# Performance work log

Measured on AMD Instinct MI355X. Metric: run time of the kernel, lower is better.

The kernel has to match this reference:

```python
import jax, jax.numpy as jnp
import numpy as np

N_PAPER, N_AUTHOR = 50000, 20000
D_IN, D_HID, N_CLS = 128, 128, 40
E_WRITES, E_CITES, E_REV = 400000, 800000, 400000
ETS = ["w", "c", "r"]  # writes(author->paper), cites(paper->paper), rev_writes(paper->author)


def setup_inputs() -> dict:
    key = jax.random.key(0)
    keys = iter(jax.random.split(key, 64))

    def nrm(shape, scale=1.0):
        return jax.random.normal(next(keys), shape, jnp.float32) * scale

    inp = {}
    inp["x_paper"] = nrm((N_PAPER, D_IN))
    inp["x_author"] = nrm((N_AUTHOR, D_IN))

    def edges(n_src, n_dst, e):
        return jnp.stack([
            jax.random.randint(next(keys), (e,), 0, n_src),
            jax.random.randint(next(keys), (e,), 0, n_dst),
        ]).astype(jnp.int32)

    inp["ei_writes"] = edges(N_AUTHOR, N_PAPER, E_WRITES)
    inp["ei_cites"] = edges(N_PAPER, N_PAPER, E_CITES)
    inp["ei_rev"] = edges(N_PAPER, N_AUTHOR, E_REV)

    # SAGEConv params per layer, per relation: W_l (neighbor lin, with bias), W_r (root lin)
    dims = [(D_IN, D_HID), (D_HID, N_CLS)]
    for l, (di, do) in enumerate(dims):
        s = 1.0 / float(np.sqrt(di))
        for e in ETS:
            inp[f"Wl{l}_{e}"] = nrm((di, do), s)
            inp[f"bl{l}_{e}"] = jnp.zeros((do,), jnp.float32)
            inp[f"Wr{l}_{e}"] = nrm((di, do), s)
    return inp


def _sage(x_src, x_dst, ei, Wl, bl, Wr, n_dst):
    # PyG SAGEConv(aggr='mean'): lin_l(mean of neighbor msgs) + lin_r(x_dst)
    msg = x_src[ei[0]]                                                    # [E, d]
    s = jax.ops.segment_sum(msg, ei[1], num_segments=n_dst)               # [n_dst, d]
    cnt = jax.ops.segment_sum(jnp.ones((ei.shape[1],), msg.dtype), ei[1],
                              num_segments=n_dst)
    agg = s / jnp.maximum(cnt, 1.0)[:, None]
    return agg @ Wl + bl + x_dst @ Wr


def reference(x_paper, x_author, ei_writes, ei_cites, ei_rev,
              Wl0_w, bl0_w, Wr0_w, Wl0_c, bl0_c, Wr0_c, Wl0_r, bl0_r, Wr0_r,
              Wl1_w, bl1_w, Wr1_w, Wl1_c, bl1_c, Wr1_c, Wl1_r, bl1_r, Wr1_r):
    def layer(hp, ha, Pw, Pc, Pr):
        out_w = _sage(ha, hp, ei_writes, *Pw, N_PAPER)   # author -> paper
        out_c = _sage(hp, hp, ei_cites, *Pc, N_PAPER)    # paper  -> paper
        out_a = _sage(hp, ha, ei_rev, *Pr, N_AUTHOR)     # paper  -> author
        # HeteroConv aggr='mean': average over relations sharing a dst type
        return 0.5 * (out_w + out_c), out_a

    hp, ha = layer(x_paper, x_author,
                   (Wl0_w, bl0_w, Wr0_w), (Wl0_c, bl0_c, Wr0_c), (Wl0_r, bl0_r, Wr0_r))
    hp, ha = jax.nn.relu(hp), jax.nn.relu(ha)  # dropout is identity at eval
    hp, ha = layer(hp, ha,
                   (Wl1_w, bl1_w, Wr1_w), (Wl1_c, bl1_c, Wr1_c), (Wl1_r, bl1_r, Wr1_r))
    return hp
```

## Files before the change

### kernel.cpp

```cpp
#include <hip/hip_runtime.h>

#define NP 50000
#define NA 20000
#define EW 400000
#define EC 800000
#define ER 400000

__global__ __launch_bounds__(256) void prep_k(
    const float* __restrict__ Wr0w, const float* __restrict__ Wr0c,
    const float* __restrict__ bl0w, const float* __restrict__ bl0c,
    const float* __restrict__ Wr1w, const float* __restrict__ Wr1c,
    const float* __restrict__ bl1w, const float* __restrict__ bl1c,
    float* __restrict__ Wr0wc, float* __restrict__ b0p,
    float* __restrict__ Wr1wc, float* __restrict__ b1p)
{
    int i = blockIdx.x * 256 + threadIdx.x;
    if (i < 128*128) Wr0wc[i] = Wr0w[i] + Wr0c[i];
    if (i < 128*40)  Wr1wc[i] = Wr1w[i] + Wr1c[i];
    if (i < 128)     b0p[i] = 0.5f*(bl0w[i] + bl0c[i]);
    if (i < 40)      b1p[i] = 0.5f*(bl1w[i] + bl1c[i]);
}

__global__ __launch_bounds__(256) void count_all_k(
    const int* __restrict__ ei_w, const int* __restrict__ ei_c, const int* __restrict__ ei_r,
    int* __restrict__ cntw, int* __restrict__ cntc, int* __restrict__ cntr)
{
    int i = blockIdx.x * 256 + threadIdx.x;
    if (i < EW)              atomicAdd(&cntw[ei_w[EW + i]], 1);
    else if (i < EW+EC)      atomicAdd(&cntc[ei_c[EC + (i-EW)]], 1);
    else if (i < EW+EC+ER)   atomicAdd(&cntr[ei_r[ER + (i-EW-EC)]], 1);
}

__global__ __launch_bounds__(1024) void scan3_k(
    int* __restrict__ c0, int n0, int* __restrict__ o0,
    int* __restrict__ c1, int n1, int* __restrict__ o1,
    int* __restrict__ c2, int n2, int* __restrict__ o2)
{
    __shared__ int sa[1024], sb[1024];
    __shared__ int carry_s;
    int* cnt; int n; int* off;
    if (blockIdx.x == 0)      { cnt = c0; n = n0; off = o0; }
    else if (blockIdx.x == 1) { cnt = c1; n = n1; off = o1; }
    else                      { cnt = c2; n = n2; off = o2; }
    const int tid = threadIdx.x;
    if (tid == 0) carry_s = 0;
    __syncthreads();
    const int nchunk = (n + 1023) / 1024;
    for (int c = 0; c < nchunk; ++c) {
        int i = c*1024 + tid;
        int v = (i < n) ? cnt[i] : 0;
        sa[tid] = v;
        __syncthreads();
        int* s = sa; int* d = sb;
        for (int sh = 1; sh < 1024; sh <<= 1) {
            int t = s[tid] + ((tid >= sh) ? s[tid - sh] : 0);
            d[tid] = t;
            __syncthreads();
            int* tmp = s; s = d; d = tmp;
        }
        int inc = s[tid];
        int carry = carry_s;
        if (i < n) off[i] = carry + inc - v;
        __syncthreads();
        if (tid == 1023) carry_s = carry + inc;
        __syncthreads();
    }
    if (tid == 0) off[n] = carry_s;
}

__global__ __launch_bounds__(256) void fill_all_k(
    const int* __restrict__ ei_w, const int* __restrict__ ei_c, const int* __restrict__ ei_r,
    const int* __restrict__ offw, const int* __restrict__ offc, const int* __restrict__ offr,
    int* __restrict__ cntw, int* __restrict__ cntc, int* __restrict__ cntr,
    int* __restrict__ adjw, int* __restrict__ adjc, int* __restrict__ adjr)
{
    int i = blockIdx.x * 256 + threadIdx.x;
    const int* ei; const int* off; int* cnt; int* adj; int e; int E;
    if (i < EW)            { e = i;        ei = ei_w; off = offw; cnt = cntw; adj = adjw; E = EW; }
    else if (i < EW+EC)    { e = i-EW;     ei = ei_c; off = offc; cnt = cntc; adj = adjc; E = EC; }
    else if (i < EW+EC+ER) { e = i-EW-EC;  ei = ei_r; off = offr; cnt = cntr; adj = adjr; E = ER; }
    else return;
    int d = ei[E + e];
    int p = atomicSub(&cnt[d], 1) - 1;
    adj[off[d] + p] = ei[e];
}

__global__ __launch_bounds__(256) void gather128_all_k(
    const float* __restrict__ x_paper, const float* __restrict__ x_author,
    const int* __restrict__ offw, const int* __restrict__ adjw, float* __restrict__ aggw,
    const int* __restrict__ offc, const int* __restrict__ adjc, float* __restrict__ aggc,
    const int* __restrict__ offr, const int* __restrict__ adjr, float* __restrict__ aggr)
{
    int W    = blockIdx.x * 4 + (threadIdx.x >> 6);
    int lane = threadIdx.x & 63;
    const float* X; const int* off; const int* adj; float* AGG; int w;
    if (W < NP)          { w = W;        X = x_author; off = offw; adj = adjw; AGG = aggw; }
    else if (W < 2*NP)   { w = W - NP;   X = x_paper;  off = offc; adj = adjc; AGG = aggc; }
    else if (W < 2*NP+NA){ w = W - 2*NP; X = x_paper;  off = offr; adj = adjr; AGG = aggr; }
    else return;
    int b = off[w], e = off[w+1];
    float2 acc = make_float2(0.f, 0.f);
    for (int j0 = b; j0 < e; j0 += 64) {
        int sl = (j0 + lane < e) ? adj[j0 + lane] : 0;
        int m  = min(64, e - j0);
        for (int k = 0; k < m; ++k) {
            int s = __shfl(sl, k, 64);
            float2 v = reinterpret_cast<const float2*>(X + (size_t)s * 128)[lane];
            acc.x += v.x; acc.y += v.y;
        }
    }
    float sc = 1.0f / fmaxf((float)(e - b), 1.0f);
    reinterpret_cast<float2*>(AGG + (size_t)w * 128)[lane] = make_float2(acc.x*sc, acc.y*sc);
}

__device__ __forceinline__ void fma4(float4& c, float a, const float4& b) {
    c.x += a*b.x; c.y += a*b.y; c.z += a*b.z; c.w += a*b.w;
}

__global__ __launch_bounds__(256) void gemmf_k(
    const float* __restrict__ A0, const float* __restrict__ A1, const float* __restrict__ A2,
    const float* __restrict__ B0, const float* __restrict__ B1, const float* __restrict__ B2,
    float* __restrict__ C, int M, int nparts, float alpha,
    const float* __restrict__ bias, int relu)
{
    __shared__ float As[32][128];
    __shared__ float Bs[32][128];
    const int tid  = threadIdx.x;
    const int row0 = blockIdx.x * 128;
    const int tx = tid & 15;
    const int ty = tid >> 4;

    float4 acc[2][2][4];
#pragma unroll
    for (int rh = 0; rh < 2; ++rh)
#pragma unroll
        for (int ch = 0; ch < 2; ++ch)
#pragma unroll
            for (int i = 0; i < 4; ++i) acc[rh][ch][i] = make_float4(0.f,0.f,0.f,0.f);

    const int KT = nparts * 4;
    for (int kt = 0; kt < KT; ++kt) {
        const int p  = kt >> 2;
        const int cb = (kt & 3) * 32;
        const float* Ap = (p == 0) ? A0 : (p == 1) ? A1 : A2;
        const float* Bp = (p == 0) ? B0 : (p == 1) ? B1 : B2;
        if (kt) __syncthreads();
#pragma unroll
        for (int i = 0; i < 4; ++i) {
            int idx = tid + i*256;
            int m = idx & 127, kq = idx >> 7;
            int row = row0 + m;
            float4 v = make_float4(0.f,0.f,0.f,0.f);
            if (row < M) v = *reinterpret_cast<const float4*>(Ap + (size_t)row*128 + cb + kq*4);
            As[kq*4+0][m] = v.x; As[kq*4+1][m] = v.y;
            As[kq*4+2][m] = v.z; As[kq*4+3][m] = v.w;
        }
#pragma unroll
        for (int i = 0; i < 4; ++i) {
            int idx = tid + i*256;
            int n4 = idx & 31, k = idx >> 5;
            *reinterpret_cast<float4*>(&Bs[k][n4*4]) =
                *reinterpret_cast<const float4*>(Bp + (size_t)(cb + k)*128 + n4*4);
        }
        __syncthreads();
#pragma unroll 8
        for (int k = 0; k < 32; ++k) {
            float4 a0 = *reinterpret_cast<const float4*>(&As[k][ty*4]);
            float4 a1 = *reinterpret_cast<const float4*>(&As[k][64 + ty*4]);
            float4 b0 = *reinterpret_cast<const float4*>(&Bs[k][tx*4]);
            float4 b1 = *reinterpret_cast<const float4*>(&Bs[k][64 + tx*4]);
#pragma unroll
            for (int i = 0; i < 4; ++i) {
                float av = (&a0.x)[i];
                fma4(acc[0][0][i], av, b0);
                fma4(acc[0][1][i], av, b1);
            }
#pragma unroll
            for (int i = 0; i < 4; ++i) {
                float av = (&a1.x)[i];
                fma4(acc[1][0][i], av, b0);
                fma4(acc[1][1][i], av, b1);
            }
        }
    }

#pragma unroll
    for (int rh = 0; rh < 2; ++rh)
#pragma unroll
        for (int i = 0; i < 4; ++i) {
            int row = row0 + rh*64 + ty*4 + i;
            if (row >= M) continue;
#pragma unroll
            for (int ch = 0; ch < 2; ++ch) {
                int col = ch*64 + tx*4;
                float4 t = acc[rh][ch][i];
                float4 bb = *reinterpret_cast<const float4*>(&bias[col]);
                t.x = alpha*t.x + bb.x; t.y = alpha*t.y + bb.y;
                t.z = alpha*t.z + bb.z; t.w = alpha*t.w + bb.w;
                if (relu) {
                    t.x = fmaxf(t.x, 0.f); t.y = fmaxf(t.y, 0.f);
                    t.z = fmaxf(t.z, 0.f); t.w = fmaxf(t.w, 0.f);
                }
                *reinterpret_cast<float4*>(C + (size_t)row*128 + col) = t;
            }
        }
}

__global__ __launch_bounds__(256) void gemm40_k(
    const float* __restrict__ A, const float* __restrict__ B, float* __restrict__ C, int M)
{
    __shared__ float Bs[128][40];
    __shared__ float As[24][128];
    const int tid  = threadIdx.x;
    const int row0 = blockIdx.x * 24;

#pragma unroll
    for (int i = 0; i < 5; ++i) {
        int idx = tid + i*256;
        reinterpret_cast<float4*>(&Bs[0][0])[idx] = reinterpret_cast<const float4*>(B)[idx];
    }
#pragma unroll
    for (int i = 0; i < 3; ++i) {
        int idx = tid + i*256;
        int r = idx >> 5, c4 = idx & 31;
        int row = row0 + r;
        float4 v = make_float4(0.f,0.f,0.f,0.f);
        if (row < M) v = reinterpret_cast<const float4*>(A + (size_t)row*128)[c4];
        reinterpret_cast<float4*>(&As[r][0])[c4] = v;
    }
    __syncthreads();

    if (tid < 240) {
        int col  = tid % 40;
        int rsub = tid / 40;
        float a0=0.f, a1=0.f, a2=0.f, a3=0.f;
        for (int k = 0; k < 128; ++k) {
            float b = Bs[k][col];
            a0 += As[rsub*4+0][k]*b;
            a1 += As[rsub*4+1][k]*b;
            a2 += As[rsub*4+2][k]*b;
            a3 += As[rsub*4+3][k]*b;
        }
        int rb = row0 + rsub*4;
        if (rb+0 < M) C[(size_t)(rb+0)*40 + col] = a0;
        if (rb+1 < M) C[(size_t)(rb+1)*40 + col] = a1;
        if (rb+2 < M) C[(size_t)(rb+2)*40 + col] = a2;
        if (rb+3 < M) C[(size_t)(rb+3)*40 + col] = a3;
    }
}

__global__ __launch_bounds__(256) void gemm40x2_k(
    const float* __restrict__ A, const float* __restrict__ B1, const float* __restrict__ B2,
    float* __restrict__ C1, float* __restrict__ C2, int M)
{
    __shared__ float Bs1[128][40];
    __shared__ float Bs2[128][40];
    __shared__ float As[24][128];
    const int tid  = threadIdx.x;
    const int row0 = blockIdx.x * 24;

#pragma unroll
    for (int i = 0; i < 5; ++i) {
        int idx = tid + i*256;
        reinterpret_cast<float4*>(&Bs1[0][0])[idx] = reinterpret_cast<const float4*>(B1)[idx];
        reinterpret_cast<float4*>(&Bs2[0][0])[idx] = reinterpret_cast<const float4*>(B2)[idx];
    }
#pragma unroll
    for (int i = 0; i < 3; ++i) {
        int idx = tid + i*256;
        int r = idx >> 5, c4 = idx & 31;
        int row = row0 + r;
        float4 v = make_float4(0.f,0.f,0.f,0.f);
        if (row < M) v = reinterpret_cast<const float4*>(A + (size_t)row*128)[c4];
        reinterpret_cast<float4*>(&As[r][0])[c4] = v;
    }
    __syncthreads();

    if (tid < 240) {
        int col  = tid % 40;
        int rsub = tid / 40;
        float p0=0.f,p1=0.f,p2=0.f,p3=0.f;
        float q0=0.f,q1=0.f,q2=0.f,q3=0.f;
        for (int k = 0; k < 128; ++k) {
            float b1 = Bs1[k][col];
            float b2 = Bs2[k][col];
            float v0 = As[rsub*4+0][k], v1 = As[rsub*4+1][k];
            float v2 = As[rsub*4+2][k], v3 = As[rsub*4+3][k];
            p0 += v0*b1; p1 += v1*b1; p2 += v2*b1; p3 += v3*b1;
            q0 += v0*b2; q1 += v1*b2; q2 += v2*b2; q3 += v3*b2;
        }
        int rb = row0 + rsub*4;
        if (rb+0 < M) { C1[(size_t)(rb+0)*40 + col] = p0; C2[(size_t)(rb+0)*40 + col] = q0; }
        if (rb+1 < M) { C1[(size_t)(rb+1)*40 + col] = p1; C2[(size_t)(rb+1)*40 + col] = q1; }
        if (rb+2 < M) { C1[(size_t)(rb+2)*40 + col] = p2; C2[(size_t)(rb+2)*40 + col] = q2; }
        if (rb+3 < M) { C1[(size_t)(rb+3)*40 + col] = p3; C2[(size_t)(rb+3)*40 + col] = q3; }
    }
}

__global__ __launch_bounds__(256) void gather40f_k(
    const float* __restrict__ T1w, const float* __restrict__ T1c,
    const int* __restrict__ offw, const int* __restrict__ adjw,
    const int* __restrict__ offc, const int* __restrict__ adjc,
    const float* __restrict__ b1p, float* __restrict__ out)
{
    int w    = blockIdx.x * 4 + (threadIdx.x >> 6);
    int lane = threadIdx.x & 63;
    if (w >= NP) return;
    const bool act = lane < 40;

    float aw = 0.f;
    {
        int b = offw[w], e = offw[w+1];
        for (int j0 = b; j0 < e; j0 += 64) {
            int sl = (j0 + lane < e) ? adjw[j0 + lane] : 0;
            int m  = min(64, e - j0);
            for (int k = 0; k < m; ++k) {
                int s = __shfl(sl, k, 64);
                if (act) aw += T1w[(size_t)s * 40 + lane];
            }
        }
        aw *= 1.0f / fmaxf((float)(e - b), 1.0f);
    }
    float ac = 0.f;
    {
        int b = offc[w], e = offc[w+1];
        for (int j0 = b; j0 < e; j0 += 64) {
            int sl = (j0 + lane < e) ? adjc[j0 + lane] : 0;
            int m  = min(64, e - j0);
            for (int k = 0; k < m; ++k) {
                int s = __shfl(sl, k, 64);
                if (act) ac += T1c[(size_t)s * 40 + lane];
            }
        }
        ac *= 1.0f / fmaxf((float)(e - b), 1.0f);
    }
    if (act) {
        size_t idx = (size_t)w * 40 + lane;
        out[idx] = 0.5f*(aw + ac + out[idx]) + b1p[lane];
    }
}

extern "C" void kernel_launch(void* const* d_in, const int* in_sizes, int n_in,
                              void* d_out, int out_size, void* d_ws, size_t ws_size,
                              hipStream_t stream)
{
    (void)in_sizes; (void)n_in; (void)out_size; (void)ws_size;

    const float* x_paper  = (const float*)d_in[0];
    const float* x_author = (const float*)d_in[1];
    const int*   ei_w     = (const int*)d_in[2];
    const int*   ei_c     = (const int*)d_in[3];
    const int*   ei_r     = (const int*)d_in[4];
    const float* Wl0w = (const float*)d_in[5];
    const float* bl0w = (const float*)d_in[6];
    const float* Wr0w = (const float*)d_in[7];
    const float* Wl0c = (const float*)d_in[8];
    const float* bl0c = (const float*)d_in[9];
    const float* Wr0c = (const float*)d_in[10];
    const float* Wl0r = (const float*)d_in[11];
    const float* bl0r = (const float*)d_in[12];
    const float* Wr0r = (const float*)d_in[13];
    const float* Wl1w = (const float*)d_in[14];
    const float* bl1w = (const float*)d_in[15];
    const float* Wr1w = (const float*)d_in[16];
    const float* Wl1c = (const float*)d_in[17];
    const float* bl1c = (const float*)d_in[18];
    const float* Wr1c = (const float*)d_in[19];
    float* out = (float*)d_out;

    float* ws = (float*)d_ws;
    size_t o = 0;
    int* cntw = (int*)(ws + o); o += NP;
    int* cntc = (int*)(ws + o); o += NP;
    int* cntr = (int*)(ws + o); o += NA;
    const size_t zeroInts = o;
    int* offw = (int*)(ws + o); o += NP + 1;
    int* offc = (int*)(ws + o); o += NP + 1;
    int* offr = (int*)(ws + o); o += NA + 1;
    o = (o + 3) & ~(size_t)3;
    int* adjw = (int*)(ws + o); o += EW;
    int* adjc = (int*)(ws + o); o += EC;
    int* adjr = (int*)(ws + o); o += ER;
    float* aggw = ws + o; o += (size_t)NP*128;
    float* aggc = ws + o; o += (size_t)NP*128;
    float* aggr = ws + o; o += (size_t)NA*128;
    float* hp1  = ws + o; o += (size_t)NP*128;
    float* ha1  = ws + o; o += (size_t)NA*128;
    float* Wr0wc = ws + o; o += 128*128;
    float* b0p   = ws + o; o += 128;
    float* Wr1wc = ws + o; o += 128*40;
    float* b1p   = ws + o; o += 40;
    float* T1w   = aggw;
    float* T1c   = aggw + (size_t)NA*40;

    hipMemsetAsync(d_ws, 0, zeroInts * sizeof(int), stream);

    prep_k<<<64, 256, 0, stream>>>(Wr0w, Wr0c, bl0w, bl0c, Wr1w, Wr1c, bl1w, bl1c,
                                   Wr0wc, b0p, Wr1wc, b1p);

    count_all_k<<<(EW+EC+ER+255)/256, 256, 0, stream>>>(ei_w, ei_c, ei_r, cntw, cntc, cntr);
    scan3_k<<<3, 1024, 0, stream>>>(cntw, NP, offw, cntc, NP, offc, cntr, NA, offr);
    fill_all_k<<<(EW+EC+ER+255)/256, 256, 0, stream>>>(ei_w, ei_c, ei_r, offw, offc, offr,
                                                       cntw, cntc, cntr, adjw, adjc, adjr);

    gather128_all_k<<<(2*NP+NA+3)/4, 256, 0, stream>>>(x_paper, x_author,
                                                       offw, adjw, aggw,
                                                       offc, adjc, aggc,
                                                       offr, adjr, aggr);

    gemmf_k<<<(NP+127)/128, 256, 0, stream>>>(x_paper, aggw, aggc, Wr0wc, Wl0w, Wl0c,
                                              hp1, NP, 3, 0.5f, b0p, 1);
    gemmf_k<<<(NA+127)/128, 256, 0, stream>>>(x_author, aggr, nullptr, Wr0r, Wl0r, nullptr,
                                              ha1, NA, 2, 1.0f, bl0r, 1);

    gemm40_k  <<<(NA+23)/24, 256, 0, stream>>>(ha1, Wl1w, T1w, NA);
    gemm40x2_k<<<(NP+23)/24, 256, 0, stream>>>(hp1, Wl1c, Wr1wc, T1c, out, NP);

    gather40f_k<<<(NP+3)/4, 256, 0, stream>>>(T1w, T1c, offw, adjw, offc, adjc, b1p, out);
}
```

Before: 721.1 us.

## Use wave-shuffle scan in CSR offsets and register-prefetch GEMM tiles

The single-block-per-relation prefix scan now handles 4096 elements per chunk with int4 loads, wave-level shuffle scans and a small cross-wave scan. This replaces the 10-step shared-memory Hillis-Steele scan that synchronized the block at every step. Offset arrays are padded so that vector stores stay 16-byte aligned. The dense GEMM now prefetches the next k-tile from global memory into registers while computing the current tile, which hides load latency at the cost of extra registers and an extra barrier.

```diff
diff --git a/kernel.cpp b/kernel.cpp
--- a/kernel.cpp
+++ b/kernel.cpp
@@ -32,37 +32,66 @@
 }
 
 __global__ __launch_bounds__(1024) void scan3_k(
-    int* __restrict__ c0, int n0, int* __restrict__ o0,
-    int* __restrict__ c1, int n1, int* __restrict__ o1,
-    int* __restrict__ c2, int n2, int* __restrict__ o2)
-{
-    __shared__ int sa[1024], sb[1024];
+    const int* __restrict__ c0, int n0, int* __restrict__ o0,
+    const int* __restrict__ c1, int n1, int* __restrict__ o1,
+    const int* __restrict__ c2, int n2, int* __restrict__ o2)
+{
+    __shared__ int wsum[16];
     __shared__ int carry_s;
-    int* cnt; int n; int* off;
+    const int* cnt; int n; int* off;
     if (blockIdx.x == 0)      { cnt = c0; n = n0; off = o0; }
     else if (blockIdx.x == 1) { cnt = c1; n = n1; off = o1; }
     else                      { cnt = c2; n = n2; off = o2; }
-    const int tid = threadIdx.x;
+    const int tid  = threadIdx.x;
+    const int lane = tid & 63;
+    const int wid  = tid >> 6;
     if (tid == 0) carry_s = 0;
     __syncthreads();
-    const int nchunk = (n + 1023) / 1024;
+    const int CH = 4096;
+    const int nchunk = (n + CH - 1) / CH;
     for (int c = 0; c < nchunk; ++c) {
-        int i = c*1024 + tid;
-        int v = (i < n) ? cnt[i] : 0;
-        sa[tid] = v;
+        int base = c*CH + tid*4;
+        int4 v = make_int4(0,0,0,0);
+        if (base + 3 < n) v = *reinterpret_cast<const int4*>(cnt + base);
+        else {
+            if (base   < n) v.x = cnt[base];
+            if (base+1 < n) v.y = cnt[base+1];
+            if (base+2 < n) v.z = cnt[base+2];
+            if (base+3 < n) v.w = cnt[base+3];
+        }
+        int s1 = v.x + v.y, s2 = s1 + v.z, s3 = s2 + v.w;
+        int x = s3;
+#pragma unroll
+        for (int d = 1; d < 64; d <<= 1) {
+            int u = __shfl_up(x, d, 64);
+            if (lane >= d) x += u;
+        }
+        if (lane == 63) wsum[wid] = x;
+        int texc = x - s3;
         __syncthreads();
-        int* s = sa; int* d = sb;
-        for (int sh = 1; sh < 1024; sh <<= 1) {
-            int t = s[tid] + ((tid >= sh) ? s[tid - sh] : 0);
-            d[tid] = t;
-            __syncthreads();
-            int* tmp = s; s = d; d = tmp;
-        }
-        int inc = s[tid];
+        if (wid == 0 && lane < 16) {
+            int y = wsum[lane];
+#pragma unroll
+            for (int d = 1; d < 16; d <<= 1) {
+                int u = __shfl_up(y, d, 16);
+                if (lane >= d) y += u;
+            }
+            wsum[lane] = y;
+        }
+        __syncthreads();
         int carry = carry_s;
-        if (i < n) off[i] = carry + inc - v;
+        int wexc  = wid ? wsum[wid-1] : 0;
+        int pre   = carry + wexc + texc;
+        int4 ov = make_int4(pre, pre + v.x, pre + s1, pre + s2);
+        if (base + 3 < n) *reinterpret_cast<int4*>(off + base) = ov;
+        else {
+            if (base   < n) off[base]   = ov.x;
+            if (base+1 < n) off[base+1] = ov.y;
+            if (base+2 < n) off[base+2] = ov.z;
+            if (base+3 < n) off[base+3] = ov.w;
+        }
         __syncthreads();
-        if (tid == 1023) carry_s = carry + inc;
+        if (tid == 0) carry_s += wsum[15];
         __syncthreads();
     }
     if (tid == 0) off[n] = carry_s;
@@ -139,30 +168,41 @@
             for (int i = 0; i < 4; ++i) acc[rh][ch][i] = make_float4(0.f,0.f,0.f,0.f);
 
     const int KT = nparts * 4;
-    for (int kt = 0; kt < KT; ++kt) {
+    float4 ra[4], rb[4];
+
+    auto loadT = [&](int kt) {
         const int p  = kt >> 2;
         const int cb = (kt & 3) * 32;
         const float* Ap = (p == 0) ? A0 : (p == 1) ? A1 : A2;
         const float* Bp = (p == 0) ? B0 : (p == 1) ? B1 : B2;
-        if (kt) __syncthreads();
 #pragma unroll
         for (int i = 0; i < 4; ++i) {
             int idx = tid + i*256;
             int m = idx & 127, kq = idx >> 7;
             int row = row0 + m;
-            float4 v = make_float4(0.f,0.f,0.f,0.f);
-            if (row < M) v = *reinterpret_cast<const float4*>(Ap + (size_t)row*128 + cb + kq*4);
-            As[kq*4+0][m] = v.x; As[kq*4+1][m] = v.y;
-            As[kq*4+2][m] = v.z; As[kq*4+3][m] = v.w;
-        }
+            ra[i] = make_float4(0.f,0.f,0.f,0.f);
+            if (row < M) ra[i] = *reinterpret_cast<const float4*>(Ap + (size_t)row*128 + cb + kq*4);
+            int n4 = idx & 31, k = idx >> 5;
+            rb[i] = *reinterpret_cast<const float4*>(Bp + (size_t)(cb + k)*128 + n4*4);
+        }
+    };
+    auto writeT = [&]() {
 #pragma unroll
         for (int i = 0; i < 4; ++i) {
             int idx = tid + i*256;
+            int m = idx & 127, kq = idx >> 7;
+            As[kq*4+0][m] = ra[i].x; As[kq*4+1][m] = ra[i].y;
+            As[kq*4+2][m] = ra[i].z; As[kq*4+3][m] = ra[i].w;
             int n4 = idx & 31, k = idx >> 5;
-            *reinterpret_cast<float4*>(&Bs[k][n4*4]) =
-                *reinterpret_cast<const float4*>(Bp + (size_t)(cb + k)*128 + n4*4);
-        }
-        __syncthreads();
+            *reinterpret_cast<float4*>(&Bs[k][n4*4]) = rb[i];
+        }
+    };
+
+    loadT(0);
+    writeT();
+    __syncthreads();
+    for (int kt = 0; kt < KT; ++kt) {
+        if (kt + 1 < KT) loadT(kt + 1);
 #pragma unroll 8
         for (int k = 0; k < 32; ++k) {
             float4 a0 = *reinterpret_cast<const float4*>(&As[k][ty*4]);
@@ -181,6 +221,11 @@
                 fma4(acc[1][0][i], av, b0);
                 fma4(acc[1][1][i], av, b1);
             }
+        }
+        if (kt + 1 < KT) {
+            __syncthreads();
+            writeT();
+            __syncthreads();
         }
     }
 
@@ -374,10 +419,9 @@
     int* cntc = (int*)(ws + o); o += NP;
     int* cntr = (int*)(ws + o); o += NA;
     const size_t zeroInts = o;
-    int* offw = (int*)(ws + o); o += NP + 1;
-    int* offc = (int*)(ws + o); o += NP + 1;
-    int* offr = (int*)(ws + o); o += NA + 1;
-    o = (o + 3) & ~(size_t)3;
+    int* offw = (int*)(ws + o); o += NP + 4;
+    int* offc = (int*)(ws + o); o += NP + 4;
+    int* offr = (int*)(ws + o); o += NA + 4;
     int* adjw = (int*)(ws + o); o += EW;
     int* adjc = (int*)(ws + o); o += EC;
     int* adjr = (int*)(ws + o); o += ER;
```

Result: slower. 749.7 us (+4.0%).
